# Performance work log

Hardware: AMD Instinct MI355X
Metric: run time of the kernel (lower is better)

## Reference

```python
import jax, jax.numpy as jnp
import numpy as np

B, T, C, H = 4, 1024, 1024, 16
D = C // H  # head dim = 64


def setup_inputs() -> dict:
    key = jax.random.key(0)
    ks = jax.random.split(key, 12)
    s = 1.0 / np.sqrt(C)
    inp = {
        "x": jax.random.normal(ks[0], (B, T, C), jnp.float32),
        "Wq": jax.random.normal(ks[1], (C, C), jnp.float32) * s,
        "bq": jnp.zeros((C,), jnp.float32),
        "Wk": jax.random.normal(ks[2], (C, C), jnp.float32) * s,
        "bk": jnp.zeros((C,), jnp.float32),
        "Wv": jax.random.normal(ks[3], (C, C), jnp.float32) * s,
        "bv": jnp.zeros((C,), jnp.float32),
        "time_weighting": jnp.ones((H, T, T), jnp.float32),
        "head_mix_w": jax.random.normal(ks[4], (H, H), jnp.float32) * (1.0 / np.sqrt(H)),
        "Wp": jax.random.normal(ks[5], (C, C), jnp.float32) * s,
        "bp": jnp.zeros((C,), jnp.float32),
    }
    return inp


def reference(x, Wq, bq, Wk, bk, Wv, bv, time_weighting, head_mix_w, Wp, bp):
    Bx, Tx, Cx = x.shape
    half = Cx // 2
    # time_shift: first half of channels sees x shifted by one step (row 0 -> zeros)
    x_shift = jnp.pad(x, ((0, 0), (1, 0), (0, 0)))[:, :Tx, :half]
    xs = jnp.concatenate([x_shift, x[:, :, half:]], axis=-1)

    def heads(y):  # [B,T,C] -> [B,H,T,D]
        return y.reshape(Bx, Tx, H, D).transpose(0, 2, 1, 3)

    q = heads(xs @ Wq.T + bq)
    k = heads(xs @ Wk.T + bk)
    v = heads(xs @ Wv.T + bv)

    att = jnp.einsum("bhtd,bhsd->bhts", q, k) * (1.0 / np.sqrt(D))
    causal = jnp.tril(jnp.ones((Tx, Tx), bool))
    att = jnp.where(causal, att, -jnp.inf)
    att = jax.nn.softmax(att, axis=-1)
    att = att * time_weighting[:, :Tx, :Tx]
    # 1x1 conv across heads
    att = jnp.einsum("oh,bhts->bots", head_mix_w, att)

    y = jnp.einsum("bhts,bhsd->bhtd", att, v)
    y = y.transpose(0, 2, 1, 3).reshape(Bx, Tx, Cx)
    return y @ Wp.T + bp
```

## Files before the change

kernel.cpp:

```cpp
#include <hip/hip_runtime.h>
#include <hip/hip_bf16.h>

#define T_ 1024

typedef __attribute__((ext_vector_type(8))) short short8;
typedef __attribute__((ext_vector_type(4))) float f32x4;
typedef __bf16 bf16x8 __attribute__((ext_vector_type(8)));
typedef _Float16 f16x8 __attribute__((ext_vector_type(8)));
typedef _Float16 f16x4 __attribute__((ext_vector_type(4)));
typedef __attribute__((ext_vector_type(4))) unsigned short ushort4v;

__device__ __forceinline__ unsigned short f2bf(float f) {
    unsigned u = __float_as_uint(f);
    u += 0x7fffu + ((u >> 16) & 1u);
    return (unsigned short)(u >> 16);
}
__device__ __forceinline__ float bf2f(unsigned short s) {
    return __uint_as_float(((unsigned)s) << 16);
}
__device__ __forceinline__ unsigned short f2h(float f) {
    _Float16 h = (_Float16)f;
    return __builtin_bit_cast(unsigned short, h);
}
__device__ __forceinline__ float h2f(unsigned short u) {
    return (float)__builtin_bit_cast(_Float16, u);
}

__global__ __launch_bounds__(256) void k_convert(
    const float* __restrict__ s0, const float* __restrict__ s1,
    const float* __restrict__ s2, const float* __restrict__ s3,
    unsigned short* __restrict__ d0, unsigned short* __restrict__ d1,
    unsigned short* __restrict__ d2, unsigned short* __restrict__ d3) {
    const float* src; unsigned short* dst;
    switch (blockIdx.y) {
        case 0:  src = s0; dst = d0; break;
        case 1:  src = s1; dst = d1; break;
        case 2:  src = s2; dst = d2; break;
        default: src = s3; dst = d3; break;
    }
    int i = (blockIdx.x * 256 + threadIdx.x) * 4;
    float4 v = *(const float4*)(src + i);
    ushort4v ov = { f2bf(v.x), f2bf(v.y), f2bf(v.z), f2bf(v.w) };
    *(ushort4v*)(dst + i) = ov;
}

__global__ __launch_bounds__(256) void k_xs(const float* __restrict__ x,
                                            unsigned short* __restrict__ xs) {
    int idx = (blockIdx.x * 256 + threadIdx.x) * 4;
    int c = idx & 1023;
    int m = idx >> 10;
    int t = m & 1023;
    float4 v;
    if (c < 512) {
        if (t == 0) { v.x = v.y = v.z = v.w = 0.f; }
        else        { v = *(const float4*)(x + (size_t)(m - 1) * 1024 + c); }
    } else {
        v = *(const float4*)(x + (size_t)m * 1024 + c);
    }
    ushort4v ov = { f2bf(v.x), f2bf(v.y), f2bf(v.z), f2bf(v.w) };
    *(ushort4v*)(xs + (size_t)m * 1024 + c) = ov;
}

__device__ __forceinline__ void gemm_body(const unsigned short* __restrict__ A,
                                          const unsigned short* __restrict__ Bt,
                                          int m0, int n0, int tid, f32x4 acc[4][4],
                                          unsigned short (*As)[32], unsigned short (*Bs)[32]) {
    const int lane = tid & 63, w = tid >> 6;
    const int wr = w >> 1, wc = w & 1;
#pragma unroll
    for (int i = 0; i < 4; i++)
#pragma unroll
        for (int j = 0; j < 4; j++) acc[i][j] = (f32x4){0.f, 0.f, 0.f, 0.f};

    for (int k0 = 0; k0 < 1024; k0 += 32) {
        __syncthreads();
#pragma unroll
        for (int it = 0; it < 2; it++) {
            int ch = it * 256 + tid;
            int row = ch >> 2, c = ch & 3;
            int col = (c ^ ((row >> 1) & 3)) * 8;
            *(short8*)&As[row][col] = *(const short8*)(A + (size_t)(m0 + row) * 1024 + k0 + c * 8);
            *(short8*)&Bs[row][col] = *(const short8*)(Bt + (size_t)(n0 + row) * 1024 + k0 + c * 8);
        }
        __syncthreads();
        bf16x8 af[4], bg[4];
        int c = lane >> 4;
#pragma unroll
        for (int i = 0; i < 4; i++) {
            int row = wr * 64 + i * 16 + (lane & 15);
            af[i] = *(const bf16x8*)&As[row][(c ^ ((row >> 1) & 3)) * 8];
        }
#pragma unroll
        for (int j = 0; j < 4; j++) {
            int row = wc * 64 + j * 16 + (lane & 15);
            bg[j] = *(const bf16x8*)&Bs[row][(c ^ ((row >> 1) & 3)) * 8];
        }
#pragma unroll
        for (int i = 0; i < 4; i++)
#pragma unroll
            for (int j = 0; j < 4; j++)
                acc[i][j] = __builtin_amdgcn_mfma_f32_16x16x32_bf16(af[i], bg[j], acc[i][j], 0, 0, 0);
    }
}

__global__ __launch_bounds__(256) void k_gemm_qkv(
    const unsigned short* __restrict__ A,
    const unsigned short* __restrict__ wq, const unsigned short* __restrict__ wk,
    const unsigned short* __restrict__ wv,
    const float* __restrict__ bq, const float* __restrict__ bk, const float* __restrict__ bv,
    unsigned short* __restrict__ qo, unsigned short* __restrict__ ko,
    unsigned short* __restrict__ vo) {
    __shared__ unsigned short As[128][32];
    __shared__ unsigned short Bs[128][32];
    const int mat = blockIdx.y >> 3;
    const unsigned short* Bt = mat == 0 ? wq : (mat == 1 ? wk : wv);
    const float* bias = mat == 0 ? bq : (mat == 1 ? bk : bv);
    unsigned short* out = mat == 0 ? qo : (mat == 1 ? ko : vo);
    const int m0 = blockIdx.x * 128, n0 = (blockIdx.y & 7) * 128;
    const int tid = threadIdx.x, lane = tid & 63, w = tid >> 6;
    const int wr = w >> 1, wc = w & 1;
    f32x4 acc[4][4];
    gemm_body(A, Bt, m0, n0, tid, acc, As, Bs);
#pragma unroll
    for (int i = 0; i < 4; i++) {
        int mbase = m0 + wr * 64 + i * 16 + ((lane >> 4) << 2);
#pragma unroll
        for (int j = 0; j < 4; j++) {
            int n = n0 + wc * 64 + j * 16 + (lane & 15);
            float bv_ = bias[n];
            int h = n >> 6, d = n & 63;
#pragma unroll
            for (int r = 0; r < 4; r++) {
                int mm = mbase + r;
                int b = mm >> 10, t = mm & 1023;
                out[(size_t)((b * 16 + h) * 1024 + t) * 64 + d] = f2bf(acc[i][j][r] + bv_);
            }
        }
    }
}

__global__ __launch_bounds__(256) void k_gemm_out(
    const unsigned short* __restrict__ A, const unsigned short* __restrict__ Bt,
    const float* __restrict__ bias, float* __restrict__ out) {
    __shared__ unsigned short As[128][32];
    __shared__ unsigned short Bs[128][32];
    const int m0 = blockIdx.x * 128, n0 = blockIdx.y * 128;
    const int tid = threadIdx.x, lane = tid & 63, w = tid >> 6;
    const int wr = w >> 1, wc = w & 1;
    f32x4 acc[4][4];
    gemm_body(A, Bt, m0, n0, tid, acc, As, Bs);
#pragma unroll
    for (int i = 0; i < 4; i++) {
        int mbase = m0 + wr * 64 + i * 16 + ((lane >> 4) << 2);
#pragma unroll
        for (int j = 0; j < 4; j++) {
            int n = n0 + wc * 64 + j * 16 + (lane & 15);
            float bv_ = bias[n];
#pragma unroll
            for (int r = 0; r < 4; r++)
                out[(size_t)(mbase + r) * 1024 + n] = acc[i][j][r] + bv_;
        }
    }
}

__global__ __launch_bounds__(256) void k_scores(const unsigned short* __restrict__ qb,
                                                const unsigned short* __restrict__ kb,
                                                unsigned short* __restrict__ Eb,
                                                float* __restrict__ invb) {
    __shared__ unsigned short qs[64][64];
    __shared__ unsigned short ks[64][64];
    const int tid = threadIdx.x, lane = tid & 63, w = tid >> 6;
    const int t0 = (15 - (int)blockIdx.x) * 64;
    const int bh = blockIdx.y;
    const unsigned short* qp = qb + (size_t)bh * 65536;
    const unsigned short* kp = kb + (size_t)bh * 65536;

#pragma unroll
    for (int it = 0; it < 2; it++) {
        int ch = it * 256 + tid; int row = ch >> 3, c = ch & 7;
        *(short8*)&qs[row][(c ^ (row & 7)) * 8] = *(const short8*)(qp + (size_t)(t0 + row) * 64 + c * 8);
    }
    __syncthreads();
    const int row_a = w * 16 + (lane & 15);
    bf16x8 a0 = *(const bf16x8*)&qs[row_a][(((lane >> 4)    ) ^ (row_a & 7)) * 8];
    bf16x8 a1 = *(const bf16x8*)&qs[row_a][(((lane >> 4) + 4) ^ (row_a & 7)) * 8];
    const int tr = t0 + w * 16 + ((lane >> 4) << 2);
    float l_[4] = {0.f, 0.f, 0.f, 0.f};
    unsigned short* ep = Eb + (size_t)bh * ((size_t)T_ * T_);

    for (int s0 = 0; s0 <= t0 + 63; s0 += 64) {
        __syncthreads();
#pragma unroll
        for (int it = 0; it < 2; it++) {
            int ch = it * 256 + tid; int row = ch >> 3, c = ch & 7;
            *(short8*)&ks[row][(c ^ (row & 7)) * 8] = *(const short8*)(kp + (size_t)(s0 + row) * 64 + c * 8);
        }
        __syncthreads();
        f32x4 S[4];
#pragma unroll
        for (int sf = 0; sf < 4; sf++) {
            int row = sf * 16 + (lane & 15);
            bf16x8 b0 = *(const bf16x8*)&ks[row][(((lane >> 4)    ) ^ (row & 7)) * 8];
            bf16x8 b1 = *(const bf16x8*)&ks[row][(((lane >> 4) + 4) ^ (row & 7)) * 8];
            f32x4 z = (f32x4){0.f, 0.f, 0.f, 0.f};
            z = __builtin_amdgcn_mfma_f32_16x16x32_bf16(a0, b0, z, 0, 0, 0);
            z = __builtin_amdgcn_mfma_f32_16x16x32_bf16(a1, b1, z, 0, 0, 0);
            S[sf] = z;
        }
#pragma unroll
        for (int sf = 0; sf < 4; sf++) {
            int s = s0 + sf * 16 + (lane & 15);
#pragma unroll
            for (int r = 0; r < 4; r++) {
                float es = (s <= tr + r) ? __expf(S[sf][r] * 0.125f) : 0.f;
                l_[r] += es;
                ep[(size_t)(tr + r) * T_ + s] = f2h(es);
            }
        }
    }
#pragma unroll
    for (int r = 0; r < 4; r++) {
        float ts = l_[r];
        ts += __shfl_xor(ts, 1);
        ts += __shfl_xor(ts, 2);
        ts += __shfl_xor(ts, 4);
        ts += __shfl_xor(ts, 8);
        l_[r] = ts;
    }
    if ((lane & 15) == 0) {
#pragma unroll
        for (int r = 0; r < 4; r++) invb[(size_t)bh * T_ + tr + r] = 1.f / l_[r];
    }
}

__global__ __launch_bounds__(256) void k_mix3(unsigned short* __restrict__ Sb,
                                              const float* __restrict__ invb,
                                              const float* __restrict__ tw,
                                              const float* __restrict__ mixw) {
    const int t = blockIdx.x, b = blockIdx.y;
    const int send = t | 63;
    const int tid = threadIdx.x, lane = tid & 63, w = tid >> 6;
    __shared__ unsigned short p2[1024][24];
    __shared__ float inv_s[16];
    if (tid < 16) inv_s[tid] = invb[(size_t)(b * 16 + tid) * T_ + t];
    __syncthreads();

    unsigned short* plane0 = Sb + (size_t)b * 16 * 1048576;
    const int s4 = tid * 4;
    if (s4 <= send) {
        const unsigned rowb = (unsigned)t * 1024u + (unsigned)s4;
        unsigned short ph[4][16];
#pragma unroll
        for (int h = 0; h < 16; h++) {
            ushort4v e4 = *(const ushort4v*)(plane0 + (size_t)h * 1048576 + rowb);
            float4 t4 = *(const float4*)(tw + (size_t)h * 1048576 + rowb);
            float iv = inv_s[h];
            ph[0][h] = f2h(h2f(e4.x) * iv * t4.x);
            ph[1][h] = f2h(h2f(e4.y) * iv * t4.y);
            ph[2][h] = f2h(h2f(e4.z) * iv * t4.z);
            ph[3][h] = f2h(h2f(e4.w) * iv * t4.w);
        }
#pragma unroll
        for (int j = 0; j < 4; j++) {
            *(short8*)&p2[s4 + j][0] = *(short8*)&ph[j][0];
            *(short8*)&p2[s4 + j][8] = *(short8*)&ph[j][8];
        }
    }

    f16x4 af;
#pragma unroll
    for (int j = 0; j < 4; j++)
        af[j] = (_Float16)mixw[(lane & 15) * 16 + (lane >> 4) * 4 + j];
    __syncthreads();

    const int ng = (send + 1) >> 4;
    const unsigned obase = (unsigned)t * 1024u;
    for (int g = w; g < ng; g += 4) {
        int pos = g * 16 + (lane & 15);
        f16x4 bf = *(const f16x4*)&p2[pos][(lane >> 4) * 4];
        f32x4 d = __builtin_amdgcn_mfma_f32_16x16x16f16(af, bf, (f32x4){0.f, 0.f, 0.f, 0.f}, 0, 0, 0);
#pragma unroll
        for (int r = 0; r < 4; r++) {
            int o = (lane >> 4) * 4 + r;
            plane0[(size_t)o * 1048576 + obase + pos] = f2bf(d[r]);
        }
    }
}

__global__ __launch_bounds__(256) void k_av(const unsigned short* __restrict__ att,
                                            const unsigned short* __restrict__ vb,
                                            unsigned short* __restrict__ y1) {
    __shared__ unsigned short as_[64][64];
    __shared__ unsigned short vs[64][72];
    const int tid = threadIdx.x, lane = tid & 63, w = tid >> 6;
    const int t0 = (15 - (int)blockIdx.x) * 64;
    const int bh = blockIdx.y;
    const int b = bh >> 4, h = bh & 15;
    const unsigned short* ap = att + (size_t)bh * 1048576;
    const unsigned short* vp = vb + (size_t)bh * 65536;
    f32x4 acc[4];
#pragma unroll
    for (int j = 0; j < 4; j++) acc[j] = (f32x4){0.f, 0.f, 0.f, 0.f};

    for (int s0 = 0; s0 <= t0 + 63; s0 += 64) {
        __syncthreads();
#pragma unroll
        for (int it = 0; it < 2; it++) {
            int ch = it * 256 + tid;
            int row = ch >> 3, c = ch & 7;
            *(short8*)&as_[row][(c ^ (row & 7)) * 8] =
                *(const short8*)(ap + (size_t)(t0 + row) * 1024 + s0 + c * 8);
            int sp = ch >> 3, dc = (ch & 7) * 8;
            short8 vv = *(const short8*)(vp + (size_t)(s0 + sp) * 64 + dc);
#pragma unroll
            for (int i = 0; i < 8; i++) vs[dc + i][sp] = ((unsigned short*)&vv)[i];
        }
        __syncthreads();
        const int row_a = w * 16 + (lane & 15);
#pragma unroll
        for (int ks = 0; ks < 2; ks++) {
            bf16x8 af = *(const bf16x8*)&as_[row_a][((((lane >> 4) + 4 * ks)) ^ (row_a & 7)) * 8];
#pragma unroll
            for (int j = 0; j < 4; j++) {
                bf16x8 bg = *(const bf16x8*)&vs[j * 16 + (lane & 15)][ks * 32 + (lane >> 4) * 8];
                acc[j] = __builtin_amdgcn_mfma_f32_16x16x32_bf16(af, bg, acc[j], 0, 0, 0);
            }
        }
    }

    int t = t0 + w * 16 + ((lane >> 4) << 2);
#pragma unroll
    for (int j = 0; j < 4; j++) {
        int d = j * 16 + (lane & 15);
#pragma unroll
        for (int r = 0; r < 4; r++)
            y1[(size_t)(b * 1024 + t + r) * 1024 + h * 64 + d] = f2bf(acc[j][r]);
    }
}

extern "C" void kernel_launch(void* const* d_in, const int* in_sizes, int n_in,
                              void* d_out, int out_size, void* d_ws, size_t ws_size,
                              hipStream_t stream) {
    (void)in_sizes; (void)n_in; (void)out_size; (void)ws_size;
    const float* x    = (const float*)d_in[0];
    const float* Wq   = (const float*)d_in[1];
    const float* bq   = (const float*)d_in[2];
    const float* Wk   = (const float*)d_in[3];
    const float* bk   = (const float*)d_in[4];
    const float* Wv   = (const float*)d_in[5];
    const float* bv   = (const float*)d_in[6];
    const float* tw   = (const float*)d_in[7];
    const float* mixw = (const float*)d_in[8];
    const float* Wp   = (const float*)d_in[9];
    const float* bp   = (const float*)d_in[10];

    char* ws = (char*)d_ws;
    size_t off = 0;
    auto alloc = [&](size_t bytes) -> char* {
        char* p = ws + off;
        off += (bytes + 255) & ~(size_t)255;
        return p;
    };
    unsigned short* xs  = (unsigned short*)alloc((size_t)4096 * 1024 * 2);
    unsigned short* wqb = (unsigned short*)alloc((size_t)1024 * 1024 * 2);
    unsigned short* wkb = (unsigned short*)alloc((size_t)1024 * 1024 * 2);
    unsigned short* wvb = (unsigned short*)alloc((size_t)1024 * 1024 * 2);
    unsigned short* wpb = (unsigned short*)alloc((size_t)1024 * 1024 * 2);
    unsigned short* qb  = (unsigned short*)alloc((size_t)64 * 1024 * 64 * 2);
    unsigned short* kb  = (unsigned short*)alloc((size_t)64 * 1024 * 64 * 2);
    unsigned short* vb_ = (unsigned short*)alloc((size_t)64 * 1024 * 64 * 2);
    unsigned short* Sb  = (unsigned short*)alloc((size_t)64 * 1024 * 1024 * 2);
    float*          invb = (float*)alloc((size_t)64 * 1024 * 4);
    unsigned short* y1  = (unsigned short*)alloc((size_t)4096 * 1024 * 2);

    k_convert<<<dim3(1024, 4), 256, 0, stream>>>(Wq, Wk, Wv, Wp, wqb, wkb, wvb, wpb);
    k_xs<<<4096, 256, 0, stream>>>(x, xs);
    k_gemm_qkv<<<dim3(32, 24), 256, 0, stream>>>(xs, wqb, wkb, wvb, bq, bk, bv, qb, kb, vb_);
    k_scores<<<dim3(16, 64), 256, 0, stream>>>(qb, kb, Sb, invb);
    k_mix3<<<dim3(1024, 4), 256, 0, stream>>>(Sb, invb, tw, mixw);
    k_av<<<dim3(16, 64), 256, 0, stream>>>(Sb, vb_, y1);
    k_gemm_out<<<dim3(32, 8), 256, 0, stream>>>(y1, wpb, bp, (float*)d_out);
}
```

Baseline: 333.9 us.

## Use direct global-to-LDS loads in GEMM and vectorize mix-kernel stores

The shared GEMM body now stages A/B tiles with global_load_lds 16-byte loads straight into LDS. The loads keep the XOR swizzle by permuting the global chunk each lane fetches, so they no longer pass through registers. The head-mix kernel swaps its MFMA operands so each lane holds four consecutive positions of one output head, and writes them as a single 8-byte packed store instead of four scattered 2-byte stores. The LDS staging row padding shrinks from 24 to 18 halves, which leaves the 36-byte row stride unaligned for the vector LDS reads and writes.

```diff
diff --git a/kernel.cpp b/kernel.cpp
--- a/kernel.cpp
+++ b/kernel.cpp
@@ -24,6 +24,12 @@
 }
 __device__ __forceinline__ float h2f(unsigned short u) {
     return (float)__builtin_bit_cast(_Float16, u);
+}
+
+__device__ __forceinline__ void gload16(const unsigned short* g, unsigned short* l) {
+    __builtin_amdgcn_global_load_lds((const __attribute__((address_space(1))) unsigned int*)g,
+                                     (__attribute__((address_space(3))) unsigned int*)l,
+                                     16, 0, 0);
 }
 
 __global__ __launch_bounds__(256) void k_convert(
@@ -67,6 +73,8 @@
                                           unsigned short (*As)[32], unsigned short (*Bs)[32]) {
     const int lane = tid & 63, w = tid >> 6;
     const int wr = w >> 1, wc = w & 1;
+    const int srow = lane >> 2;
+    const int scp  = lane & 3;
 #pragma unroll
     for (int i = 0; i < 4; i++)
 #pragma unroll
@@ -76,11 +84,11 @@
         __syncthreads();
 #pragma unroll
         for (int it = 0; it < 2; it++) {
-            int ch = it * 256 + tid;
-            int row = ch >> 2, c = ch & 3;
-            int col = (c ^ ((row >> 1) & 3)) * 8;
-            *(short8*)&As[row][col] = *(const short8*)(A + (size_t)(m0 + row) * 1024 + k0 + c * 8);
-            *(short8*)&Bs[row][col] = *(const short8*)(Bt + (size_t)(n0 + row) * 1024 + k0 + c * 8);
+            int base = it * 64 + w * 16;
+            int row = base + srow;
+            int c2 = scp ^ ((row >> 1) & 3);
+            gload16(A + (size_t)(m0 + row) * 1024 + k0 + c2 * 8, &As[base][0]);
+            gload16(Bt + (size_t)(n0 + row) * 1024 + k0 + c2 * 8, &Bs[base][0]);
         }
         __syncthreads();
         bf16x8 af[4], bg[4];
@@ -233,14 +241,14 @@
     }
 }
 
-__global__ __launch_bounds__(256) void k_mix3(unsigned short* __restrict__ Sb,
+__global__ __launch_bounds__(256) void k_mix4(unsigned short* __restrict__ Sb,
                                               const float* __restrict__ invb,
                                               const float* __restrict__ tw,
                                               const float* __restrict__ mixw) {
     const int t = blockIdx.x, b = blockIdx.y;
     const int send = t | 63;
     const int tid = threadIdx.x, lane = tid & 63, w = tid >> 6;
-    __shared__ unsigned short p2[1024][24];
+    __shared__ unsigned short p2[1024][18];
     __shared__ float inv_s[16];
     if (tid < 16) inv_s[tid] = invb[(size_t)(b * 16 + tid) * T_ + t];
     __syncthreads();
@@ -267,23 +275,20 @@
         }
     }
 
-    f16x4 af;
+    f16x4 bmix;
 #pragma unroll
     for (int j = 0; j < 4; j++)
-        af[j] = (_Float16)mixw[(lane & 15) * 16 + (lane >> 4) * 4 + j];
+        bmix[j] = (_Float16)mixw[(lane & 15) * 16 + (lane >> 4) * 4 + j];
     __syncthreads();
 
     const int ng = (send + 1) >> 4;
     const unsigned obase = (unsigned)t * 1024u;
+    const int o = lane & 15;
     for (int g = w; g < ng; g += 4) {
-        int pos = g * 16 + (lane & 15);
-        f16x4 bf = *(const f16x4*)&p2[pos][(lane >> 4) * 4];
-        f32x4 d = __builtin_amdgcn_mfma_f32_16x16x16f16(af, bf, (f32x4){0.f, 0.f, 0.f, 0.f}, 0, 0, 0);
-#pragma unroll
-        for (int r = 0; r < 4; r++) {
-            int o = (lane >> 4) * 4 + r;
-            plane0[(size_t)o * 1048576 + obase + pos] = f2bf(d[r]);
-        }
+        f16x4 af = *(const f16x4*)&p2[g * 16 + (lane & 15)][(lane >> 4) * 4];
+        f32x4 d = __builtin_amdgcn_mfma_f32_16x16x16f16(af, bmix, (f32x4){0.f, 0.f, 0.f, 0.f}, 0, 0, 0);
+        ushort4v pk = { f2bf(d[0]), f2bf(d[1]), f2bf(d[2]), f2bf(d[3]) };
+        *(ushort4v*)(plane0 + (size_t)o * 1048576 + obase + g * 16 + ((lane >> 4) << 2)) = pk;
     }
 }
 
@@ -377,7 +382,7 @@
     k_xs<<<4096, 256, 0, stream>>>(x, xs);
     k_gemm_qkv<<<dim3(32, 24), 256, 0, stream>>>(xs, wqb, wkb, wvb, bq, bk, bv, qb, kb, vb_);
     k_scores<<<dim3(16, 64), 256, 0, stream>>>(qb, kb, Sb, invb);
-    k_mix3<<<dim3(1024, 4), 256, 0, stream>>>(Sb, invb, tw, mixw);
+    k_mix4<<<dim3(1024, 4), 256, 0, stream>>>(Sb, invb, tw, mixw);
     k_av<<<dim3(16, 64), 256, 0, stream>>>(Sb, vb_, y1);
     k_gemm_out<<<dim3(32, 8), 256, 0, stream>>>(y1, wpb, bp, (float*)d_out);
 }
```

New measurement: 328.3 us. About the same (-1.7%).
